# Performance work log

Hardware: AMD Instinct MI355X
Metric: run time of the kernel (lower is better)

The kernel has to match this reference:

```python
import jax, jax.numpy as jnp
from jax import lax
import numpy as np

B, T, C = 4, 2048, 1024
H = 4                      # num_heads
D = C // H                 # head_dim
EPS_N = 1e-6               # normalizer eps in scan
EPS_GN = 1e-5              # GroupNorm eps (torch default)


def setup_inputs() -> dict:
    key = jax.random.key(0)
    ks = jax.random.split(key, 8)
    s = 0.02
    return {
        "x": jax.random.normal(ks[0], (B, T, C), jnp.float32),
        "conv_w": jax.random.normal(ks[1], (C, 1, 4), jnp.float32) * s,
        "conv_b": jax.random.normal(ks[2], (C,), jnp.float32) * s,
        "wx_w": jax.random.normal(ks[3], (4 * C, C), jnp.float32) * s,
        "wx_b": jax.random.normal(ks[4], (4 * C,), jnp.float32) * s,
        "gn_w": jnp.ones((C,), jnp.float32),
        "gn_b": jnp.zeros((C,), jnp.float32),
        "out_w": jax.random.normal(ks[5], (C, C), jnp.float32) * s,
        "out_b": jax.random.normal(ks[6], (C,), jnp.float32) * s,
    }


def _slstm_scan(i_g, f_g, z_g, o_g):
    # all inputs (B,T,H,D); scan over time
    def step(carry, g):
        c, n, m = carry
        i_t, f_t, z_t, o_t = g
        m_t = jnp.maximum(f_t + m, i_t)
        i_p = jnp.exp(i_t - m_t)
        f_p = jnp.exp(f_t + m - m_t)
        c_t = f_p * c + i_p * z_t
        n_t = f_p * n + i_p
        h_t = jax.nn.sigmoid(o_t) * (c_t / (n_t + EPS_N))
        return (c_t, n_t, m_t), h_t

    tfirst = lambda a: jnp.transpose(a, (1, 0, 2, 3))  # (T,B,H,D)
    init = (jnp.zeros((B, H, D), i_g.dtype),
            jnp.ones((B, H, D), i_g.dtype),
            jnp.zeros((B, H, D), i_g.dtype))
    _, h_seq = lax.scan(step, init, (tfirst(i_g), tfirst(f_g), tfirst(z_g), tfirst(o_g)))
    return jnp.transpose(h_seq, (1, 0, 2, 3))  # (B,T,H,D)


def reference(x, conv_w, conv_b, wx_w, wx_b, gn_w, gn_b, out_w, out_b):
    # causal depthwise conv (torch pad=3 both sides, sliced to first T == left pad 3)
    xc = jnp.transpose(x, (0, 2, 1))  # (B,C,T)
    xc = lax.conv_general_dilated(
        xc, conv_w, window_strides=(1,), padding=[(3, 0)],
        dimension_numbers=("NCH", "OIH", "NCH"), feature_group_count=C)
    xc = jax.nn.silu(xc + conv_b[None, :, None])
    xc = jnp.transpose(xc, (0, 2, 1))  # (B,T,C)

    gates = jnp.einsum("btc,gc->btg", xc, wx_w) + wx_b  # (B,T,4C)
    gates = gates.reshape(B, T, 4, H, D)
    i_g, f_g, z_g, o_g = (gates[:, :, k] for k in range(4))
    z_g = jnp.tanh(z_g)

    h = _slstm_scan(i_g, f_g, z_g, o_g).reshape(B, T, C)

    # GroupNorm(H groups) over (B,C,T): normalize per (batch, group) over (D, T)
    hg = h.reshape(B, T, H, D)
    mean = hg.mean(axis=(1, 3), keepdims=True)
    var = hg.var(axis=(1, 3), keepdims=True)
    hn = ((hg - mean) / jnp.sqrt(var + EPS_GN)).reshape(B, T, C)
    hn = hn * gn_w + gn_b

    out = jnp.einsum("btc,oc->bto", hn, out_w) + out_b
    return out + x  # dropout is identity at inference
```

## Files before the change

kernel.cpp:

```cpp
#include <hip/hip_runtime.h>

#define B_ 4
#define T_ 2048
#define C_ 1024
#define H_ 4
#define D_ 256
#define M_ (B_*T_)
#define N1_ (4*C_)
#define K_ C_
#define LANES_ (B_*C_)
#define CHUNK_ 32
#define NCHUNK_ (T_/CHUNK_)

typedef unsigned short u16;
typedef unsigned int u32;
typedef __bf16 bf16x8 __attribute__((ext_vector_type(8)));
typedef float f32x4 __attribute__((ext_vector_type(4)));
typedef float vf4 __attribute__((ext_vector_type(4)));
typedef unsigned short u16x4 __attribute__((ext_vector_type(4)));
typedef unsigned short u16x8 __attribute__((ext_vector_type(8)));

__device__ __forceinline__ u16 f2bf(float f) {
  union { float f; u32 u; } v; v.f = f;
  u32 u = v.u;
  u32 r = (u + 0x7FFFu + ((u >> 16) & 1u)) >> 16;
  return (u16)r;
}
__device__ __forceinline__ float b2f(u16 h) {
  union { u32 u; float f; } v; v.u = ((u32)h) << 16;
  return v.f;
}

#define NCAST_ ((N1_*K_ + C_*C_) / 2048)

__global__ void prep_kernel(const float* __restrict__ wx_w, const float* __restrict__ out_w,
                            u16* __restrict__ w1p, u16* __restrict__ w2,
                            const float* __restrict__ x, const float* __restrict__ cw,
                            const float* __restrict__ cb, u16* __restrict__ xc,
                            float* __restrict__ stats) {
  if (blockIdx.x < NCAST_) {
    int i8 = (blockIdx.x * 256 + threadIdx.x) * 8;
    u16x8 o;
    if (i8 < N1_ * K_) {
      int n = i8 >> 10, k8 = i8 & 1023;
      const float* src = wx_w + (size_t)(((n & 3) << 10) | (n >> 2)) * K_ + k8;
      vf4 a = *(const vf4*)src;
      vf4 b = *(const vf4*)(src + 4);
#pragma unroll
      for (int j = 0; j < 4; ++j) { o[j] = f2bf(a[j]); o[j + 4] = f2bf(b[j]); }
      *(u16x8*)(w1p + i8) = o;
    } else {
      int j8 = i8 - N1_ * K_;
      vf4 a = *(const vf4*)(out_w + j8);
      vf4 b = *(const vf4*)(out_w + j8 + 4);
#pragma unroll
      for (int j = 0; j < 4; ++j) { o[j] = f2bf(a[j]); o[j + 4] = f2bf(b[j]); }
      *(u16x8*)(w2 + j8) = o;
    }
    return;
  }
  if (blockIdx.x == NCAST_ && threadIdx.x < 32) stats[threadIdx.x] = 0.f;
  int i4 = ((blockIdx.x - NCAST_) * 256 + threadIdx.x) * 4;
  int c = i4 & (C_ - 1);
  int t = (i4 >> 10) & (T_ - 1);
  vf4 acc = *(const vf4*)(cb + c);
  vf4 w0 = *(const vf4*)(cw + (size_t)c * 4);
  vf4 w1 = *(const vf4*)(cw + (size_t)(c + 1) * 4);
  vf4 w2v = *(const vf4*)(cw + (size_t)(c + 2) * 4);
  vf4 w3 = *(const vf4*)(cw + (size_t)(c + 3) * 4);
#pragma unroll
  for (int k = 0; k < 4; ++k) {
    if (t - 3 + k >= 0) {
      vf4 xv = *(const vf4*)(x + (size_t)i4 + (size_t)(k - 3) * C_);
      acc[0] = fmaf(w0[k], xv[0], acc[0]);
      acc[1] = fmaf(w1[k], xv[1], acc[1]);
      acc[2] = fmaf(w2v[k], xv[2], acc[2]);
      acc[3] = fmaf(w3[k], xv[3], acc[3]);
    }
  }
  u16x4 o;
#pragma unroll
  for (int j = 0; j < 4; ++j) {
    float s = acc[j] / (1.f + __expf(-acc[j]));
    o[j] = f2bf(s);
  }
  *(u16x4*)(xc + i4) = o;
}


__device__ __forceinline__ void stage32(const u16* __restrict__ G, int rowBase, int ks,
                                        u16* dstPart, int wave, int lane) {
#pragma unroll
  for (int r = 0; r < 2; ++r) {
    int R = r * 64 + wave * 8 + (lane >> 3);
    int c = (lane & 7) ^ (R & 7);
    int grow = 2 * R + (c >> 2);
    int koff = ks * 32 + (c & 3) * 8;
    const u16* src = G + (size_t)(rowBase + grow) * K_ + koff;
    __builtin_amdgcn_global_load_lds(
        (const __attribute__((address_space(1))) u32*)src,
        (__attribute__((address_space(3))) u32*)&dstPart[(r * 64 + wave * 8) * 64],
        16, 0, 0);
  }
}

#define BAR() __builtin_amdgcn_s_barrier()

#define VM8 asm volatile("s_waitcnt vmcnt(8)" ::: "memory")
#define VM4 asm volatile("s_waitcnt vmcnt(4)" ::: "memory")
#define VM0 asm volatile("s_waitcnt vmcnt(0)" ::: "memory")
#define VMNONE ((void)0)

#define GEMM_SLICE(sIdx, DO_STAGE, VMW) do {                                     \
    u16* base_ = smem + ((sIdx) & 3) * 16384;                                    \
    const u16* aP_ = base_;                                                      \
    const u16* bP_ = base_ + 8192;                                               \
    bf16x8 af_[4], bf_[4];                                                       \
    _Pragma("unroll")                                                            \
    for (int sub = 0; sub < 4; ++sub) {                                          \
      int ra = wr * 128 + sub * 16 + l15;                                        \
      int Ra = ra >> 1;                                                          \
      int ca = (((ra & 1) << 2) | q) ^ (Ra & 7);                                 \
      af_[sub] = *(const bf16x8*)&aP_[Ra * 64 + ca * 8];                         \
      int rb = wc * 64 + sub * 16 + l15;                                         \
      int Rb = rb >> 1;                                                          \
      int cb = (((rb & 1) << 2) | q) ^ (Rb & 7);                                 \
      bf_[sub] = *(const bf16x8*)&bP_[Rb * 64 + cb * 8];                         \
    }                                                                            \
    if (DO_STAGE) stage32(A, bm, (sIdx) + 3,                                     \
        smem + (((sIdx) + 3) & 3) * 16384, wave, lane);                          \
    BAR();                                                                       \
    __builtin_amdgcn_s_setprio(1);                                               \
    _Pragma("unroll")                                                            \
    for (int sm = 0; sm < 4; ++sm)                                               \
      _Pragma("unroll")                                                          \
      for (int sn = 0; sn < 4; ++sn)                                             \
        acc[sm][sn] = __builtin_amdgcn_mfma_f32_16x16x32_bf16(af_[sm], bf_[sn],  \
                                                              acc[sm][sn], 0, 0, 0); \
    __builtin_amdgcn_s_setprio(0);                                               \
    BAR();                                                                       \
    _Pragma("unroll")                                                            \
    for (int sub = 0; sub < 4; ++sub) {                                          \
      int ra = wr * 128 + 64 + sub * 16 + l15;                                   \
      int Ra = ra >> 1;                                                          \
      int ca = (((ra & 1) << 2) | q) ^ (Ra & 7);                                 \
      af_[sub] = *(const bf16x8*)&aP_[Ra * 64 + ca * 8];                         \
    }                                                                            \
    if (DO_STAGE) stage32(Bw, bn, (sIdx) + 3,                                    \
        smem + (((sIdx) + 3) & 3) * 16384 + 8192, wave, lane);                   \
    BAR();                                                                       \
    __builtin_amdgcn_s_setprio(1);                                               \
    _Pragma("unroll")                                                            \
    for (int sm = 0; sm < 4; ++sm)                                               \
      _Pragma("unroll")                                                          \
      for (int sn = 0; sn < 4; ++sn)                                             \
        acc[4 + sm][sn] = __builtin_amdgcn_mfma_f32_16x16x32_bf16(af_[sm], bf_[sn], \
                                                          acc[4 + sm][sn], 0, 0, 0); \
    __builtin_amdgcn_s_setprio(0);                                               \
    VMW;                                                                         \
    BAR();                                                                       \
  } while (0)

__global__ __launch_bounds__(512, 2)
void gemm256_gates(const u16* __restrict__ A, const u16* __restrict__ Bw,
                   const float* __restrict__ bias,
                   u16* __restrict__ obf, f32x4* __restrict__ sSum)
{
  __shared__ __align__(16) u16 smem[67584];

  const int tid  = threadIdx.x;
  const int lane = tid & 63;
  const int l15  = lane & 15;
  const int q    = lane >> 4;
  const int wave = tid >> 6;
  const int wr   = wave >> 2;
  const int wc   = wave & 3;

  const int bid = blockIdx.y * 16 + blockIdx.x;
  const int swz = (bid & 7) * 64 + (bid >> 3);
  const int bm = (swz >> 4) * 256;
  const int bn = (swz & 15) * 256;

  float bias4[4];
#pragma unroll
  for (int sn = 0; sn < 4; ++sn) {
    int gcol = bn + wc * 64 + sn * 16 + l15;
    bias4[sn] = bias[((gcol & 3) << 10) | (gcol >> 2)];
  }
  const bool zlane = ((l15 & 3) == 2);

  f32x4 acc[8][4];
#pragma unroll
  for (int i = 0; i < 8; ++i)
#pragma unroll
    for (int j = 0; j < 4; ++j) acc[i][j] = (f32x4){0.f, 0.f, 0.f, 0.f};

#pragma unroll
  for (int s3 = 0; s3 < 3; ++s3) {
    stage32(A,  bm, s3, smem + s3 * 16384,        wave, lane);
    stage32(Bw, bn, s3, smem + s3 * 16384 + 8192, wave, lane);
  }
  asm volatile("s_waitcnt vmcnt(8)" ::: "memory");
  BAR();

#pragma unroll 1
  for (int s = 0; s < 29; ++s) GEMM_SLICE(s, true, VM8);
  GEMM_SLICE(29, false, VM4);
  GEMM_SLICE(30, false, VM0);
  GEMM_SLICE(31, false, VMNONE);

#pragma unroll
  for (int sm = 0; sm < 8; ++sm) {
#pragma unroll
    for (int r = 0; r < 4; ++r) {
      int lrow = wr * 128 + sm * 16 + q * 4 + r;
#pragma unroll
      for (int sn = 0; sn < 4; ++sn) {
        int lcol = wc * 64 + sn * 16 + l15;
        float v = acc[sm][sn][r] + bias4[sn];
        if (zlane) {
          float e = __expf(2.f * v);
          v = (e - 1.f) / (e + 1.f);
        }
        smem[lrow * 264 + lcol] = f2bf(v);
      }
    }
  }
  __syncthreads();

#pragma unroll
  for (int it = 0; it < 16; ++it) {
    int flat = it * 512 + tid;
    int row = flat >> 5;
    int ch8 = flat & 31;
    u16x8 vv = *(const u16x8*)&smem[row * 264 + ch8 * 8];
    *(u16x8*)(obf + (size_t)(bm + row) * N1_ + bn + ch8 * 8) = vv;
  }

  {
    int ch = tid & 63, ck = tid >> 6;
    const u16* sp = smem + (ck * 32) * 264 + ch * 4;
    float F = 0.f, Mx = -1e30f, aBc = 0.f, aBn = 0.f;
#pragma unroll 8
    for (int t = 0; t < CHUNK_; ++t) {
      u16x4 gv = *(const u16x4*)(sp + t * 264);
      float i_t = b2f(gv[0]), f_t = b2f(gv[1]), z_t = b2f(gv[2]);
      float Mf = Mx + f_t;
      float Mn = fmaxf(Mf, i_t);
      float ea = __expf(Mf - Mn), eb = __expf(i_t - Mn);
      aBc = ea * aBc + eb * z_t;
      aBn = ea * aBn + eb;
      F += f_t; Mx = Mn;
    }
    int b = bm >> 11;
    int s_ = ((bm & 2047) >> 5) + ck;
    int cg = (bn >> 2) + ch;
    sSum[(size_t)s_ * LANES_ + b * C_ + cg] = (f32x4){F, Mx, aBc, aBn};
  }
}

template <int EPI>
__global__ __launch_bounds__(256, 3)
void gemm_bt(const u16* __restrict__ A, const u16* __restrict__ Bw,
             const float* __restrict__ bias, const float* __restrict__ resid,
             u16* __restrict__ obf, float* __restrict__ of32,
             f32x4* __restrict__ sSum, int M, int N, int K)
{
  __shared__ __align__(16) u16 smem[128 * 136];
  u16* a_s = smem;
  u16* b_s = smem + 128 * 64;

  const int tid  = threadIdx.x;
  const int lane = tid & 63;
  const int l15  = lane & 15;
  const int q    = lane >> 4;
  const int wave = tid >> 6;
  const int wm   = (wave >> 1) * 64;
  const int wn   = (wave & 1) * 64;
  const int bm   = blockIdx.y * 128;
  const int bn   = blockIdx.x * 128;

  const int srow   = wave * 8 + (lane >> 3);
  const int schunk = lane & 7;

  float bias4[4];
#pragma unroll
  for (int sn = 0; sn < 4; ++sn) {
    int gcol = bn + wn + sn * 16 + l15;
    bias4[sn] = (EPI == 0) ? bias[((gcol & 3) << 10) | (gcol >> 2)] : bias[gcol];
  }
  const bool zlane = (EPI == 0) && ((l15 & 3) == 2);

  f32x4 acc[4][4];
#pragma unroll
  for (int i = 0; i < 4; ++i)
#pragma unroll
    for (int j = 0; j < 4; ++j) acc[i][j] = (f32x4){0.f, 0.f, 0.f, 0.f};

  for (int k0 = 0; k0 < K; k0 += 64) {
#pragma unroll
    for (int i = 0; i < 4; ++i) {
      int r = i * 32 + srow;
      int lc = schunk ^ (r & 7);
      const u16* ga = A  + (size_t)(bm + r) * K + k0 + lc * 8;
      const u16* gb = Bw + (size_t)(bn + r) * K + k0 + lc * 8;
      __builtin_amdgcn_global_load_lds(
          (const __attribute__((address_space(1))) u32*)ga,
          (__attribute__((address_space(3))) u32*)&a_s[(i * 32 + wave * 8) * 64],
          16, 0, 0);
      __builtin_amdgcn_global_load_lds(
          (const __attribute__((address_space(1))) u32*)gb,
          (__attribute__((address_space(3))) u32*)&b_s[(i * 32 + wave * 8) * 64],
          16, 0, 0);
    }
    __syncthreads();
#pragma unroll
    for (int kk = 0; kk < 64; kk += 32) {
      const int kc = kk >> 3;
      bf16x8 af[4], bfr[4];
#pragma unroll
      for (int s = 0; s < 4; ++s) {
        int ra = wm + s * 16 + l15;
        int ph = (kc + q) ^ (ra & 7);
        af[s] = *(const bf16x8*)&a_s[ra * 64 + ph * 8];
      }
#pragma unroll
      for (int s = 0; s < 4; ++s) {
        int rb = wn + s * 16 + l15;
        int ph = (kc + q) ^ (rb & 7);
        bfr[s] = *(const bf16x8*)&b_s[rb * 64 + ph * 8];
      }
#pragma unroll
      for (int sm = 0; sm < 4; ++sm)
#pragma unroll
        for (int sn = 0; sn < 4; ++sn)
          acc[sm][sn] = __builtin_amdgcn_mfma_f32_16x16x32_bf16(af[sm], bfr[sn], acc[sm][sn], 0, 0, 0);
    }
    __syncthreads();
  }

  if (EPI == 0) {
#pragma unroll
    for (int smi = 0; smi < 4; ++smi) {
#pragma unroll
      for (int r = 0; r < 4; ++r) {
        int lrow = wm + smi * 16 + q * 4 + r;
#pragma unroll
        for (int sni = 0; sni < 4; ++sni) {
          int lcol = wn + sni * 16 + l15;
          float v = acc[smi][sni][r] + bias4[sni];
          if (zlane) {
            float e = __expf(2.f * v);
            v = (e - 1.f) / (e + 1.f);
          }
          smem[lrow * 136 + lcol] = f2bf(v);
        }
      }
    }
    __syncthreads();
#pragma unroll
    for (int it = 0; it < 8; ++it) {
      int flat = it * 256 + tid;
      int row = flat >> 4;
      int ch  = flat & 15;
      u16x8 vv = *(const u16x8*)&smem[row * 136 + ch * 8];
      *(u16x8*)(obf + (size_t)(bm + row) * N + bn + ch * 8) = vv;
    }
    if (tid < 128) {
      int ch = tid & 31, ck = tid >> 5;
      const u16* sp = smem + (ck * 32) * 136 + ch * 4;
      float F = 0.f, Mx = -1e30f, aBc = 0.f, aBn = 0.f;
#pragma unroll 8
      for (int t = 0; t < CHUNK_; ++t) {
        u16x4 gv = *(const u16x4*)(sp + t * 136);
        float i_t = b2f(gv[0]), f_t = b2f(gv[1]), z_t = b2f(gv[2]);
        float Mf = Mx + f_t;
        float Mn = fmaxf(Mf, i_t);
        float ea = __expf(Mf - Mn), eb = __expf(i_t - Mn);
        aBc = ea * aBc + eb * z_t;
        aBn = ea * aBn + eb;
        F += f_t; Mx = Mn;
      }
      int b = bm >> 11;
      int s = ((bm & 2047) >> 5) + ck;
      int cg = (bn >> 2) + ch;
      sSum[(size_t)s * LANES_ + b * C_ + cg] = (f32x4){F, Mx, aBc, aBn};
    }
  } else {
    float* fs = (float*)smem;
#pragma unroll
    for (int h = 0; h < 2; ++h) {
      __syncthreads();
#pragma unroll
      for (int smi2 = 0; smi2 < 2; ++smi2) {
        int smi = 2 * h + smi2;
#pragma unroll
        for (int r = 0; r < 4; ++r) {
          int slot = (wm >> 1) + smi2 * 16 + q * 4 + r;
#pragma unroll
          for (int sni = 0; sni < 4; ++sni) {
            int lcol = wn + sni * 16 + l15;
            fs[slot * 132 + lcol] = acc[smi][sni][r] + bias4[sni];
          }
        }
      }
      __syncthreads();
#pragma unroll
      for (int it = 0; it < 8; ++it) {
        int flat = it * 256 + tid;
        int slot = flat >> 5;
        int c4 = (flat & 31) * 4;
        int absrow = bm + ((slot & 32) << 1) + (h << 5) + (slot & 31);
        vf4 v = *(const vf4*)&fs[slot * 132 + c4];
        vf4 rv = *(const vf4*)(resid + (size_t)absrow * N + bn + c4);
        v[0] += rv[0]; v[1] += rv[1]; v[2] += rv[2]; v[3] += rv[3];
        *(vf4*)(of32 + (size_t)absrow * N + bn + c4) = v;
      }
    }
  }
}

__global__ void scan_prefix(const f32x4* __restrict__ sSum, f32x4* __restrict__ iSt) {
  int l = blockIdx.x * 256 + threadIdx.x;
  float ct = 0.f, nt = 1.f, mt = 0.f;
#pragma unroll 8
  for (int s = 0; s < NCHUNK_; ++s) {
    int idx = s * LANES_ + l;
    f32x4 S = sSum[idx];
    iSt[idx] = (f32x4){ct, nt, mt, 0.f};
    float mf = mt + S[0];
    float mn = fmaxf(mf, S[1]);
    float a = __expf(mf - mn);
    float bcoef = __expf(S[1] - mn);
    ct = a * ct + bcoef * S[2];
    nt = a * nt + bcoef * S[3];
    mt = mn;
  }
}

__global__ void scan_passB(const u16* __restrict__ gates, const f32x4* __restrict__ iSt,
                           u16* __restrict__ h, float* __restrict__ stats) {
  int tid = blockIdx.x * 256 + threadIdx.x;
  int lp = tid & 2047;
  int s = tid >> 11;
  int b = lp >> 9;
  int c2 = (lp & 511) * 2;
  const u16* g = gates + ((size_t)(b * T_ + s * CHUNK_) * C_ + c2) * 4;
  u16* hp = h + (size_t)(b * T_ + s * CHUNK_) * C_ + c2;
  int idx = s * LANES_ + b * C_ + c2;
  f32x4 S0 = iSt[idx], S1 = iSt[idx + 1];
  float cc0 = S0[0], nn0 = S0[1], mm0 = S0[2];
  float cc1 = S1[0], nn1 = S1[1], mm1 = S1[2];
  float ls = 0.f, lq = 0.f;
#pragma unroll 4
  for (int t = 0; t < CHUNK_; ++t) {
    u16x8 gv = *(const u16x8*)(g + (size_t)t * C_ * 4);
    float h0, h1;
    {
      float i_t = b2f(gv[0]), f_t = b2f(gv[1]), z_t = b2f(gv[2]), o_t = b2f(gv[3]);
      float m_new = fmaxf(f_t + mm0, i_t);
      float i_p = __expf(i_t - m_new);
      float f_p = __expf(f_t + mm0 - m_new);
      cc0 = f_p * cc0 + i_p * z_t;
      nn0 = f_p * nn0 + i_p;
      mm0 = m_new;
      float sig_o = 1.f / (1.f + __expf(-o_t));
      h0 = sig_o * (cc0 / (nn0 + 1e-6f));
    }
    {
      float i_t = b2f(gv[4]), f_t = b2f(gv[5]), z_t = b2f(gv[6]), o_t = b2f(gv[7]);
      float m_new = fmaxf(f_t + mm1, i_t);
      float i_p = __expf(i_t - m_new);
      float f_p = __expf(f_t + mm1 - m_new);
      cc1 = f_p * cc1 + i_p * z_t;
      nn1 = f_p * nn1 + i_p;
      mm1 = m_new;
      float sig_o = 1.f / (1.f + __expf(-o_t));
      h1 = sig_o * (cc1 / (nn1 + 1e-6f));
    }
    u16 hb0 = f2bf(h0), hb1 = f2bf(h1);
    float v0 = b2f(hb0), v1 = b2f(hb1);
    ls += v0 + v1; lq += v0 * v0 + v1 * v1;
    *(u32*)(hp + (size_t)t * C_) = (u32)hb0 | ((u32)hb1 << 16);
  }
  __shared__ float rs[256], rq[256];
  int thr = threadIdx.x;
  rs[thr] = ls; rq[thr] = lq;
  __syncthreads();
  for (int off = 64; off > 0; off >>= 1) {
    if ((thr & 127) < off) { rs[thr] += rs[thr + off]; rq[thr] += rq[thr + off]; }
    __syncthreads();
  }
  if ((thr & 127) == 0) {
    int grp = b * 4 + (c2 >> 8);
    atomicAdd(&stats[grp * 2 + 0], rs[thr]);
    atomicAdd(&stats[grp * 2 + 1], rq[thr]);
  }
}

__global__ void norm_kernel(const u16* __restrict__ h, const float* __restrict__ stats,
                            const float* __restrict__ gn_w, const float* __restrict__ gn_b,
                            u16* __restrict__ hn) {
  int i8 = (blockIdx.x * 256 + threadIdx.x) * 8;
  int c = i8 & (C_ - 1);
  int b = i8 >> 21;
  int grp = b * 4 + (c >> 8);
  const float inv_n = 1.f / (float)(T_ * D_);
  float mean = stats[grp * 2 + 0] * inv_n;
  float var  = stats[grp * 2 + 1] * inv_n - mean * mean;
  float rstd = rsqrtf(var + 1e-5f);
  u16x8 hv = *(const u16x8*)(h + i8);
  vf4 w0 = *(const vf4*)(gn_w + c), w1 = *(const vf4*)(gn_w + c + 4);
  vf4 b0 = *(const vf4*)(gn_b + c), b1 = *(const vf4*)(gn_b + c + 4);
  u16x8 o;
#pragma unroll
  for (int j = 0; j < 4; ++j) {
    o[j]     = f2bf((b2f(hv[j])     - mean) * rstd * w0[j] + b0[j]);
    o[j + 4] = f2bf((b2f(hv[j + 4]) - mean) * rstd * w1[j] + b1[j]);
  }
  *(u16x8*)(hn + i8) = o;
}

extern "C" void kernel_launch(void* const* d_in, const int* in_sizes, int n_in,
                              void* d_out, int out_size, void* d_ws, size_t ws_size,
                              hipStream_t stream) {
  const float* x      = (const float*)d_in[0];
  const float* conv_w = (const float*)d_in[1];
  const float* conv_b = (const float*)d_in[2];
  const float* wx_w   = (const float*)d_in[3];
  const float* wx_b   = (const float*)d_in[4];
  const float* gn_w   = (const float*)d_in[5];
  const float* gn_b   = (const float*)d_in[6];
  const float* out_w  = (const float*)d_in[7];
  const float* out_b  = (const float*)d_in[8];
  float* out = (float*)d_out;

  char* p = (char*)d_ws;
  u16* xc    = (u16*)p; p += (size_t)M_ * K_ * 2;
  u16* w1    = (u16*)p; p += (size_t)N1_ * K_ * 2;
  u16* w2    = (u16*)p; p += (size_t)C_ * C_ * 2;
  u16* gts   = (u16*)p; p += (size_t)M_ * N1_ * 2;
  u16* hb    = (u16*)p; p += (size_t)M_ * C_ * 2;
  u16* hn    = (u16*)p; p += (size_t)M_ * C_ * 2;
  float* stats = (float*)p; p += 256;
  const int nsum = LANES_ * NCHUNK_;
  f32x4* sSum = (f32x4*)p; p += (size_t)nsum * 16;
  f32x4* iSt  = (f32x4*)p; p += (size_t)nsum * 16;

  prep_kernel<<<NCAST_ + (M_ * C_) / 1024, 256, 0, stream>>>(
      wx_w, out_w, w1, w2, x, conv_w, conv_b, xc, stats);

  gemm256_gates<<<dim3(N1_ / 256, M_ / 256), 512, 0, stream>>>(
      xc, w1, wx_b, gts, sSum);

  scan_prefix<<<LANES_ / 256, 256, 0, stream>>>(sSum, iSt);
  scan_passB<<<(2048 * NCHUNK_) / 256, 256, 0, stream>>>(gts, iSt, hb, stats);

  norm_kernel<<<(M_ * C_) / 2048, 256, 0, stream>>>(hb, stats, gn_w, gn_b, hn);

  gemm_bt<1><<<dim3(C_ / 128, M_ / 128), 256, 0, stream>>>(
      hn, w2, out_b, x, nullptr, out, nullptr, M_, C_, K_);
}
```

Baseline: 278.9 us.

## Restructure gates GEMM main loop with one barrier per slice and register prefetch

Rewrites the K-loop of the gate GEMM. Each slice now issues all four async global-to-LDS loads at its start, runs all 32 MFMAs back to back, and takes a single barrier per slice instead of four. After that barrier it prefetches the next slice's A0 and B fragments into double-buffered registers. Staging addresses and LDS read offsets are precomputed outside the loop, and the loop is unrolled by four so buffer slots become compile-time constants. This cuts barrier and address-arithmetic overhead and overlaps LDS reads with MFMA work, at the cost of more registers in a kernel launched with occupancy 2.

```diff
diff --git a/kernel.cpp b/kernel.cpp
--- a/kernel.cpp
+++ b/kernel.cpp
@@ -88,77 +88,54 @@
 }
 
 
-__device__ __forceinline__ void stage32(const u16* __restrict__ G, int rowBase, int ks,
-                                        u16* dstPart, int wave, int lane) {
-#pragma unroll
-  for (int r = 0; r < 2; ++r) {
-    int R = r * 64 + wave * 8 + (lane >> 3);
-    int c = (lane & 7) ^ (R & 7);
-    int grow = 2 * R + (c >> 2);
-    int koff = ks * 32 + (c & 3) * 8;
-    const u16* src = G + (size_t)(rowBase + grow) * K_ + koff;
-    __builtin_amdgcn_global_load_lds(
-        (const __attribute__((address_space(1))) u32*)src,
-        (__attribute__((address_space(3))) u32*)&dstPart[(r * 64 + wave * 8) * 64],
-        16, 0, 0);
-  }
-}
-
-#define BAR() __builtin_amdgcn_s_barrier()
+#define GLL(srcp, dstp) __builtin_amdgcn_global_load_lds( \
+    (const __attribute__((address_space(1))) u32*)(srcp), \
+    (__attribute__((address_space(3))) u32*)(dstp), 16, 0, 0)
 
 #define VM8 asm volatile("s_waitcnt vmcnt(8)" ::: "memory")
 #define VM4 asm volatile("s_waitcnt vmcnt(4)" ::: "memory")
 #define VM0 asm volatile("s_waitcnt vmcnt(0)" ::: "memory")
 #define VMNONE ((void)0)
 
-#define GEMM_SLICE(sIdx, DO_STAGE, VMW) do {                                     \
-    u16* base_ = smem + ((sIdx) & 3) * 16384;                                    \
-    const u16* aP_ = base_;                                                      \
-    const u16* bP_ = base_ + 8192;                                               \
-    bf16x8 af_[4], bf_[4];                                                       \
-    _Pragma("unroll")                                                            \
-    for (int sub = 0; sub < 4; ++sub) {                                          \
-      int ra = wr * 128 + sub * 16 + l15;                                        \
-      int Ra = ra >> 1;                                                          \
-      int ca = (((ra & 1) << 2) | q) ^ (Ra & 7);                                 \
-      af_[sub] = *(const bf16x8*)&aP_[Ra * 64 + ca * 8];                         \
-      int rb = wc * 64 + sub * 16 + l15;                                         \
-      int Rb = rb >> 1;                                                          \
-      int cb = (((rb & 1) << 2) | q) ^ (Rb & 7);                                 \
-      bf_[sub] = *(const bf16x8*)&bP_[Rb * 64 + cb * 8];                         \
-    }                                                                            \
-    if (DO_STAGE) stage32(A, bm, (sIdx) + 3,                                     \
-        smem + (((sIdx) + 3) & 3) * 16384, wave, lane);                          \
-    BAR();                                                                       \
-    __builtin_amdgcn_s_setprio(1);                                               \
-    _Pragma("unroll")                                                            \
-    for (int sm = 0; sm < 4; ++sm)                                               \
-      _Pragma("unroll")                                                          \
-      for (int sn = 0; sn < 4; ++sn)                                             \
-        acc[sm][sn] = __builtin_amdgcn_mfma_f32_16x16x32_bf16(af_[sm], bf_[sn],  \
-                                                              acc[sm][sn], 0, 0, 0); \
-    __builtin_amdgcn_s_setprio(0);                                               \
-    BAR();                                                                       \
-    _Pragma("unroll")                                                            \
-    for (int sub = 0; sub < 4; ++sub) {                                          \
-      int ra = wr * 128 + 64 + sub * 16 + l15;                                   \
-      int Ra = ra >> 1;                                                          \
-      int ca = (((ra & 1) << 2) | q) ^ (Ra & 7);                                 \
-      af_[sub] = *(const bf16x8*)&aP_[Ra * 64 + ca * 8];                         \
-    }                                                                            \
-    if (DO_STAGE) stage32(Bw, bn, (sIdx) + 3,                                    \
-        smem + (((sIdx) + 3) & 3) * 16384 + 8192, wave, lane);                   \
-    BAR();                                                                       \
-    __builtin_amdgcn_s_setprio(1);                                               \
-    _Pragma("unroll")                                                            \
-    for (int sm = 0; sm < 4; ++sm)                                               \
-      _Pragma("unroll")                                                          \
-      for (int sn = 0; sn < 4; ++sn)                                             \
-        acc[4 + sm][sn] = __builtin_amdgcn_mfma_f32_16x16x32_bf16(af_[sm], bf_[sn], \
-                                                          acc[4 + sm][sn], 0, 0, 0); \
-    __builtin_amdgcn_s_setprio(0);                                               \
-    VMW;                                                                         \
-    BAR();                                                                       \
+#define SLICE_BODY(sIdx, SLOT, P, DO_STAGE, VMW, DO_NEXT) do {                \
+    if (DO_STAGE) {                                                           \
+      u16* dp_ = smem + (((SLOT) + 3) & 3) * 16384;                           \
+      GLL(aSrc0 + ((sIdx) + 3) * 32, dp_ + dOff0);                            \
+      GLL(aSrc1 + ((sIdx) + 3) * 32, dp_ + dOff1);                            \
+      GLL(bSrc0 + ((sIdx) + 3) * 32, dp_ + 8192 + dOff0);                     \
+      GLL(bSrc1 + ((sIdx) + 3) * 32, dp_ + 8192 + dOff1);                     \
+    }                                                                         \
+    {                                                                         \
+      const u16* cb_ = smem + (SLOT) * 16384;                                 \
+      _Pragma("unroll")                                                       \
+      for (int sub = 0; sub < 4; ++sub)                                       \
+        af1[sub] = *(const bf16x8*)(cb_ + offA1[sub]);                        \
+    }                                                                         \
+    __builtin_amdgcn_s_setprio(1);                                            \
+    _Pragma("unroll")                                                         \
+    for (int sm = 0; sm < 4; ++sm)                                            \
+      _Pragma("unroll")                                                       \
+      for (int sn = 0; sn < 4; ++sn)                                          \
+        acc[sm][sn] = __builtin_amdgcn_mfma_f32_16x16x32_bf16(af0[P][sm],     \
+                          bfb[P][sn], acc[sm][sn], 0, 0, 0);                  \
+    _Pragma("unroll")                                                         \
+    for (int sm = 0; sm < 4; ++sm)                                            \
+      _Pragma("unroll")                                                       \
+      for (int sn = 0; sn < 4; ++sn)                                          \
+        acc[4 + sm][sn] = __builtin_amdgcn_mfma_f32_16x16x32_bf16(af1[sm],    \
+                          bfb[P][sn], acc[4 + sm][sn], 0, 0, 0);              \
+    __builtin_amdgcn_s_setprio(0);                                            \
+    VMW;                                                                      \
+    if (DO_NEXT) {                                                            \
+      __builtin_amdgcn_s_barrier();                                           \
+      asm volatile("" ::: "memory");                                          \
+      const u16* nb_ = smem + (((SLOT) + 1) & 3) * 16384;                     \
+      _Pragma("unroll")                                                       \
+      for (int sub = 0; sub < 4; ++sub) {                                     \
+        af0[1 - (P)][sub] = *(const bf16x8*)(nb_ + offA0[sub]);               \
+        bfb[1 - (P)][sub] = *(const bf16x8*)(nb_ + offB[sub]);                \
+      }                                                                       \
+    }                                                                         \
   } while (0)
 
 __global__ __launch_bounds__(512, 2)
@@ -189,25 +166,71 @@
   }
   const bool zlane = ((l15 & 3) == 2);
 
+  const int Rs0 = wave * 8 + (lane >> 3);
+  const int cs0 = (lane & 7) ^ (Rs0 & 7);
+  const int Rs1 = 64 + wave * 8 + (lane >> 3);
+  const int cs1 = (lane & 7) ^ (Rs1 & 7);
+  const u16* aSrc0 = A  + (size_t)(bm + 2 * Rs0 + (cs0 >> 2)) * K_ + (cs0 & 3) * 8;
+  const u16* aSrc1 = A  + (size_t)(bm + 2 * Rs1 + (cs1 >> 2)) * K_ + (cs1 & 3) * 8;
+  const u16* bSrc0 = Bw + (size_t)(bn + 2 * Rs0 + (cs0 >> 2)) * K_ + (cs0 & 3) * 8;
+  const u16* bSrc1 = Bw + (size_t)(bn + 2 * Rs1 + (cs1 >> 2)) * K_ + (cs1 & 3) * 8;
+  const int dOff0 = (wave * 8) * 64;
+  const int dOff1 = (64 + wave * 8) * 64;
+
+  int offA0[4], offA1[4], offB[4];
+#pragma unroll
+  for (int sub = 0; sub < 4; ++sub) {
+    int ra0 = wr * 128 + sub * 16 + l15;
+    int Ra0 = ra0 >> 1;
+    int ca0 = (((ra0 & 1) << 2) | q) ^ (Ra0 & 7);
+    offA0[sub] = Ra0 * 64 + ca0 * 8;
+    int ra1 = ra0 + 64;
+    int Ra1 = ra1 >> 1;
+    int ca1 = (((ra1 & 1) << 2) | q) ^ (Ra1 & 7);
+    offA1[sub] = Ra1 * 64 + ca1 * 8;
+    int rb = wc * 64 + sub * 16 + l15;
+    int Rb = rb >> 1;
+    int cbv = (((rb & 1) << 2) | q) ^ (Rb & 7);
+    offB[sub] = 8192 + Rb * 64 + cbv * 8;
+  }
+
   f32x4 acc[8][4];
 #pragma unroll
   for (int i = 0; i < 8; ++i)
 #pragma unroll
     for (int j = 0; j < 4; ++j) acc[i][j] = (f32x4){0.f, 0.f, 0.f, 0.f};
 
+  bf16x8 af0[2][4], bfb[2][4], af1[4];
+
 #pragma unroll
   for (int s3 = 0; s3 < 3; ++s3) {
-    stage32(A,  bm, s3, smem + s3 * 16384,        wave, lane);
-    stage32(Bw, bn, s3, smem + s3 * 16384 + 8192, wave, lane);
-  }
-  asm volatile("s_waitcnt vmcnt(8)" ::: "memory");
-  BAR();
-
-#pragma unroll 1
-  for (int s = 0; s < 29; ++s) GEMM_SLICE(s, true, VM8);
-  GEMM_SLICE(29, false, VM4);
-  GEMM_SLICE(30, false, VM0);
-  GEMM_SLICE(31, false, VMNONE);
+    u16* dp = smem + s3 * 16384;
+    GLL(aSrc0 + s3 * 32, dp + dOff0);
+    GLL(aSrc1 + s3 * 32, dp + dOff1);
+    GLL(bSrc0 + s3 * 32, dp + 8192 + dOff0);
+    GLL(bSrc1 + s3 * 32, dp + 8192 + dOff1);
+  }
+  VM8;
+  __builtin_amdgcn_s_barrier();
+  asm volatile("" ::: "memory");
+#pragma unroll
+  for (int sub = 0; sub < 4; ++sub) {
+    af0[0][sub] = *(const bf16x8*)(smem + offA0[sub]);
+    bfb[0][sub] = *(const bf16x8*)(smem + offB[sub]);
+  }
+
+  for (int s4 = 0; s4 < 28; s4 += 4) {
+    SLICE_BODY(s4 + 0, 0, 0, true, VM8, true);
+    SLICE_BODY(s4 + 1, 1, 1, true, VM8, true);
+    SLICE_BODY(s4 + 2, 2, 0, true, VM8, true);
+    SLICE_BODY(s4 + 3, 3, 1, true, VM8, true);
+  }
+  SLICE_BODY(28, 0, 0, true,  VM8,    true);
+  SLICE_BODY(29, 1, 1, false, VM4,    true);
+  SLICE_BODY(30, 2, 0, false, VM0,    true);
+  SLICE_BODY(31, 3, 1, false, VMNONE, false);
+
+  __syncthreads();
 
 #pragma unroll
   for (int sm = 0; sm < 8; ++sm) {
```

Result: slower. 285.7 us (+2.4%).
